# Kernel tuning notes

Hardware: AMD Instinct MI355X
Metric: run time of the kernel (lower is better)

The kernel has to match this reference:

```python
import jax, jax.numpy as jnp
import numpy as np

DEPTH = 4
HEADS = 8
DIM_HEAD = 32
NUM_CLUSTERS = 64
KMEANS_ITERS = 10
EPS = 1e-5


def layer_norm(x, g, b):
    m = jnp.mean(x, axis=-1, keepdims=True)
    v = jnp.var(x, axis=-1, keepdims=True)
    return (x - m) * jax.lax.rsqrt(v + EPS) * g + b


def kmeans_cluster(xf, k, iters):
    # xf: [P, D]. Lloyd's algorithm with deterministic init (first k points).
    centers = xf[:k]
    x_sq = jnp.sum(xf * xf, axis=-1, keepdims=True)  # [P,1]

    def assign(c):
        # squared distances [P, K]
        d = x_sq - 2.0 * (xf @ c.T) + jnp.sum(c * c, axis=-1)[None, :]
        return jnp.argmin(d, axis=-1)

    def step(c, _):
        labels = assign(c)
        sums = jax.ops.segment_sum(xf, labels, num_segments=k)
        counts = jax.ops.segment_sum(jnp.ones((xf.shape[0],), xf.dtype), labels, num_segments=k)
        new_c = jnp.where(counts[:, None] > 0, sums / jnp.maximum(counts, 1.0)[:, None], c)
        return new_c, None

    centers, _ = jax.lax.scan(step, centers, None, length=iters)
    labels = assign(centers)
    return centers[labels]  # gather: [P, D]


def setup_inputs() -> dict:
    key = jax.random.key(0)
    ks = jax.random.split(key, 8)
    B, N, D, L, M = 8, 1024, 256, DEPTH, 1024
    s = 0.02
    return {
        "x": jax.random.normal(ks[0], (B, N, D), jnp.float32),
        "ln1_g": jnp.ones((L, D), jnp.float32),
        "ln1_b": jnp.zeros((L, D), jnp.float32),
        "Wq": jax.random.normal(ks[1], (L, D, HEADS * DIM_HEAD), jnp.float32) * s,
        "Wkv": jax.random.normal(ks[2], (L, D, 2 * HEADS * DIM_HEAD), jnp.float32) * s,
        "Wo": jax.random.normal(ks[3], (L, HEADS * DIM_HEAD, D), jnp.float32) * s,
        "bo": jnp.zeros((L, D), jnp.float32),
        "ln2_g": jnp.ones((L, D), jnp.float32),
        "ln2_b": jnp.zeros((L, D), jnp.float32),
        "W1": jax.random.normal(ks[4], (L, D, M), jnp.float32) * s,
        "b1": jnp.zeros((L, M), jnp.float32),
        "W2": jax.random.normal(ks[5], (L, M, D), jnp.float32) * s,
        "b2": jnp.zeros((L, D), jnp.float32),
        "kW": jax.random.normal(ks[6], (D, D), jnp.float32) * s,
        "kb": jnp.zeros((D,), jnp.float32),
    }


def reference(x, ln1_g, ln1_b, Wq, Wkv, Wo, bo, ln2_g, ln2_b, W1, b1, W2, b2, kW, kb):
    B, N, D = x.shape
    h, dh = HEADS, DIM_HEAD
    scale = dh ** -0.5
    for l in range(DEPTH):
        # PreNorm self-attention + residual
        xn = layer_norm(x, ln1_g[l], ln1_b[l])
        q = (xn @ Wq[l]).reshape(B, N, h, dh)
        kv = xn @ Wkv[l]
        k, v = jnp.split(kv, 2, axis=-1)
        k = k.reshape(B, N, h, dh)
        v = v.reshape(B, N, h, dh)
        dots = jnp.einsum("bqhd,bkhd->bhqk", q, k) * scale
        attn = jax.nn.softmax(dots, axis=-1)
        out = jnp.einsum("bhqk,bkhd->bqhd", attn, v).reshape(B, N, h * dh)
        x = out @ Wo[l] + bo[l] + x
        # PreNorm FFN + residual
        xn = layer_norm(x, ln2_g[l], ln2_b[l])
        hdd = jax.nn.gelu(xn @ W1[l] + b1[l], approximate=False)
        x = hdd @ W2[l] + b2[l] + x
    # KMeans module: cluster flattened tokens, gather centers, linear transform.
    xf = x.reshape(B * N, D)
    clustered = kmeans_cluster(xf, NUM_CLUSTERS, KMEANS_ITERS)
    clustered = jax.lax.stop_gradient(clustered)  # torch detaches before sklearn
    clustered = clustered.reshape(B, N, D)
    return clustered @ kW + kb
```

## Files before the change

### kernel.cpp

```cpp
#include <hip/hip_runtime.h>
#include <hip/hip_bf16.h>
#include <math.h>

#define BN 8192
#define DMODEL 256
#define FFN 1024
#define NCLUST 64

typedef unsigned short u16;
typedef unsigned int u32;
typedef __attribute__((ext_vector_type(8))) short s16x8;
typedef __attribute__((ext_vector_type(8))) unsigned short u16x8;
typedef __attribute__((ext_vector_type(4))) unsigned short u16x4;
typedef __attribute__((ext_vector_type(4))) float f32x4;

__device__ __forceinline__ float bf2f(u16 v) {
    union { unsigned int u; float f; } w; w.u = ((unsigned int)v) << 16; return w.f;
}
__device__ __forceinline__ u16 f2bf(float f) {
    union { float f; unsigned int u; } w; w.f = f;
    unsigned int r = w.u + 0x7fffu + ((w.u >> 16) & 1u);
    return (u16)(r >> 16);
}
__device__ __forceinline__ u32 cvtpk(float lo, float hi) {
    u32 r;
    asm("v_cvt_pk_bf16_f32 %0, %1, %2" : "=v"(r) : "v"(lo), "v"(hi));
    return r;
}
__device__ __forceinline__ float u2f(u32 u) { union { u32 u; float f; } w; w.u = u; return w.f; }

__device__ __forceinline__ void gl16(const u16* g, u16* l) {
    __builtin_amdgcn_global_load_lds((const __attribute__((address_space(1))) u32*)g,
                                     (__attribute__((address_space(3))) u32*)l, 16, 0, 0);
}

#define BARRIER_LGKM() asm volatile("s_waitcnt lgkmcnt(0)\n\ts_barrier" ::: "memory")
#define MEMFENCE_ORDER() asm volatile("" ::: "memory")

__device__ __forceinline__ int sw32(int row, int col) { return row * 32 + (col ^ (((row >> 1) & 3) << 3)); }
__device__ __forceinline__ int sw64(int row, int col) { return row * 64 + (col ^ ((row & 7) << 3)); }
template<int BK>
__device__ __forceinline__ int swk(int row, int col) {
    if constexpr (BK == 32) return row * 32 + (col ^ (((row >> 1) & 3) << 3));
    else                    return row * 64 + (col ^ ((row & 7) << 3));
}

__global__ __launch_bounds__(256) void ln_wave(const float* __restrict__ x, const float* __restrict__ g,
                                               const float* __restrict__ b, u16* __restrict__ yh,
                                               u16* __restrict__ yl) {
    int t = threadIdx.x, w = t >> 6, l = t & 63;
    int row = blockIdx.x * 4 + w;
    const float* xr = x + (size_t)row * DMODEL;
    float4 v = *reinterpret_cast<const float4*>(xr + l * 4);
    float s = v.x + v.y + v.z + v.w;
    for (int off = 1; off < 64; off <<= 1) s += __shfl_xor(s, off);
    float mean = s * (1.0f / 256.0f);
    float4 dv = make_float4(v.x - mean, v.y - mean, v.z - mean, v.w - mean);
    float vs = dv.x * dv.x + dv.y * dv.y + dv.z * dv.z + dv.w * dv.w;
    for (int off = 1; off < 64; off <<= 1) vs += __shfl_xor(vs, off);
    float rs = rsqrtf(vs * (1.0f / 256.0f) + 1e-5f);
    float4 gg = *reinterpret_cast<const float4*>(g + l * 4);
    float4 bb = *reinterpret_cast<const float4*>(b + l * 4);
    float os[4] = {dv.x * rs * gg.x + bb.x, dv.y * rs * gg.y + bb.y,
                   dv.z * rs * gg.z + bb.z, dv.w * rs * gg.w + bb.w};
    u16x4 hv, lv;
#pragma unroll
    for (int j = 0; j < 4; j++) { u16 hh = f2bf(os[j]); hv[j] = hh; lv[j] = f2bf(os[j] - bf2f(hh)); }
    size_t o = (size_t)row * DMODEL + l * 4;
    *reinterpret_cast<u16x4*>(yh + o) = hv;
    *reinterpret_cast<u16x4*>(yl + o) = lv;
}

__device__ __forceinline__ void wconv_body(const float* __restrict__ W, u16* __restrict__ th,
                                           u16* __restrict__ tl, int K, int N, int bx, int by) {
    __shared__ float T[64][65];
    int k0 = by * 64, n0 = bx * 64;
    int t = threadIdx.x;
    int r = t >> 4, c4 = (t & 15) * 4;
#pragma unroll
    for (int i = 0; i < 4; i++) {
        float4 x = *reinterpret_cast<const float4*>(W + (size_t)(k0 + r + 16 * i) * N + n0 + c4);
        T[r + 16 * i][c4] = x.x; T[r + 16 * i][c4 + 1] = x.y;
        T[r + 16 * i][c4 + 2] = x.z; T[r + 16 * i][c4 + 3] = x.w;
    }
    __syncthreads();
#pragma unroll
    for (int i = 0; i < 4; i++) {
        int n = r + 16 * i;
        u16x4 h4, l4;
#pragma unroll
        for (int j = 0; j < 4; j++) {
            float v = T[c4 + j][n];
            u16 h = f2bf(v);
            h4[j] = h; l4[j] = f2bf(v - bf2f(h));
        }
        *reinterpret_cast<u16x4*>(th + (size_t)(n0 + n) * K + k0 + c4) = h4;
        *reinterpret_cast<u16x4*>(tl + (size_t)(n0 + n) * K + k0 + c4) = l4;
    }
}

__global__ __launch_bounds__(256) void wconv_all(const float* __restrict__ Wq, const float* __restrict__ Wkv,
                                                 const float* __restrict__ Wo, const float* __restrict__ W1,
                                                 const float* __restrict__ W2,
                                                 u16* __restrict__ wqkvh, u16* __restrict__ wqkvl,
                                                 u16* __restrict__ woh, u16* __restrict__ wol,
                                                 u16* __restrict__ w1h, u16* __restrict__ w1l,
                                                 u16* __restrict__ w2h, u16* __restrict__ w2l) {
    int f = blockIdx.x;
    if (f < 16)       wconv_body(Wq,  wqkvh,               wqkvl,               256, 256,  f & 3,  f >> 2);
    else if (f < 48)  { int g = f - 16;  wconv_body(Wkv, wqkvh + 65536,       wqkvl + 65536,       256, 512,  g & 7,  g >> 3); }
    else if (f < 64)  { int g = f - 48;  wconv_body(Wo,  woh,                 wol,                 256, 256,  g & 3,  g >> 2); }
    else if (f < 128) { int g = f - 64;  wconv_body(W1,  w1h,                 w1l,                 256, 1024, g & 15, g >> 4); }
    else              { int g = f - 128; wconv_body(W2,  w2h,                 w2l,                 1024, 256, g & 3,  g >> 2); }
}

template<int BM, int BNT, int BK>
__global__ __launch_bounds__(256) void gemm_t(const u16* __restrict__ Ath, const u16* __restrict__ Atl,
                                              const u16* __restrict__ Bth, const u16* __restrict__ Btl,
                                              const float* __restrict__ bias, const float* __restrict__ resid,
                                              float* __restrict__ Cf, u16* __restrict__ Ch, u16* __restrict__ Cl,
                                              int M, int N, int K, int fuse_gelu) {
    __shared__ u16 Ah[2][BM * BK], Al[2][BM * BK];
    __shared__ u16 Bh[2][BNT * BK], Bl[2][BNT * BK];
    constexpr int WAVES_N = (BM == 128 && BNT == 64) ? 1 : 2;
    constexpr int WAVES_M = 4 / WAVES_N;
    constexpr int MI = BM / (16 * WAVES_M);
    constexpr int NI = BNT / (16 * WAVES_N);
    constexpr int SEGS = (BM + BNT) * BK / 1024;
    constexpr int ROWS_SEG = 512 / BK;
    constexpr int ASEG = BM / ROWS_SEG;
    constexpr int BSEG = BNT / ROWS_SEG;
    int t = threadIdx.x;
    int m0 = blockIdx.y * BM, n0 = blockIdx.x * BNT;
    int L = t & 63, w = t >> 6, fr = L & 15, quad = L >> 4;
    int wm = (WAVES_N == 1) ? w : (w & 1);
    int wn = (WAVES_N == 1) ? 0 : (w >> 1);

    const u16* gsrc[SEGS];
    u16* ldst[SEGS];
    u32 dlt[SEGS];
    {
        int lr, lc;
        if constexpr (BK == 32) { lr = L >> 2; lc = (L & 3) * 8; }
        else                    { lr = L >> 3; lc = (L & 7) * 8; }
#pragma unroll
        for (int i = 0; i < SEGS; i++) {
            int s = w * SEGS + i;
            const u16* gb; u16* lb; int r; u32 d;
            if (s < ASEG)                 { gb = Ath + (size_t)m0 * K; lb = &Ah[0][0]; r = s * ROWS_SEG;                 d = BM * BK; }
            else if (s < 2 * ASEG)        { gb = Atl + (size_t)m0 * K; lb = &Al[0][0]; r = (s - ASEG) * ROWS_SEG;        d = BM * BK; }
            else if (s < 2 * ASEG + BSEG) { gb = Bth + (size_t)n0 * K; lb = &Bh[0][0]; r = (s - 2 * ASEG) * ROWS_SEG;    d = BNT * BK; }
            else                          { gb = Btl + (size_t)n0 * K; lb = &Bl[0][0]; r = (s - 2 * ASEG - BSEG) * ROWS_SEG; d = BNT * BK; }
            int row = r + lr;
            int scol;
            if constexpr (BK == 32) scol = lc ^ (((row >> 1) & 3) << 3);
            else                    scol = lc ^ ((row & 7) << 3);
            gsrc[i] = gb + (size_t)row * K + scol;
            ldst[i] = lb + r * BK;
            dlt[i] = d;
        }
    }

    f32x4 acc[MI][NI];
#pragma unroll
    for (int i = 0; i < MI; i++)
#pragma unroll
        for (int j = 0; j < NI; j++) acc[i][j] = (f32x4){0.0f, 0.0f, 0.0f, 0.0f};

    const int NT = K / BK;
#pragma unroll
    for (int i = 0; i < SEGS; i++) gl16(gsrc[i], ldst[i]);

    for (int tt = 0; tt < NT; tt++) {
        asm volatile("s_waitcnt lgkmcnt(0)" ::: "memory");
        __builtin_amdgcn_s_barrier();
        if (tt + 1 < NT) {
            int k0n = (tt + 1) * BK;
            u32 sel = (u32)((tt + 1) & 1);
#pragma unroll
            for (int i = 0; i < SEGS; i++) gl16(gsrc[i] + k0n, ldst[i] + sel * dlt[i]);
            asm volatile("s_waitcnt vmcnt(%0)" :: "n"(SEGS) : "memory");
        } else {
            asm volatile("s_waitcnt vmcnt(0)" ::: "memory");
        }
        __builtin_amdgcn_s_barrier();
        __builtin_amdgcn_sched_barrier(0);
        int cb = tt & 1;
        const u16* AhB = &Ah[cb][0]; const u16* AlB = &Al[cb][0];
        const u16* BhB = &Bh[cb][0]; const u16* BlB = &Bl[cb][0];
#pragma unroll
        for (int kk = 0; kk < BK / 32; kk++) {
            int kc = kk * 32 + quad * 8;
            s16x8 ah[MI], al[MI];
#pragma unroll
            for (int mi = 0; mi < MI; mi++) {
                int row = wm * (MI * 16) + mi * 16 + fr;
                ah[mi] = *reinterpret_cast<const s16x8*>(&AhB[swk<BK>(row, kc)]);
                al[mi] = *reinterpret_cast<const s16x8*>(&AlB[swk<BK>(row, kc)]);
            }
            __builtin_amdgcn_s_setprio(1);
#pragma unroll
            for (int ni = 0; ni < NI; ni++) {
                int rn = wn * (NI * 16) + ni * 16 + fr;
                s16x8 bhf = *reinterpret_cast<const s16x8*>(&BhB[swk<BK>(rn, kc)]);
                s16x8 blf = *reinterpret_cast<const s16x8*>(&BlB[swk<BK>(rn, kc)]);
#pragma unroll
                for (int mi = 0; mi < MI; mi++) {
                    acc[mi][ni] = __builtin_amdgcn_mfma_f32_16x16x32_bf16(ah[mi], bhf, acc[mi][ni], 0, 0, 0);
                    acc[mi][ni] = __builtin_amdgcn_mfma_f32_16x16x32_bf16(ah[mi], blf, acc[mi][ni], 0, 0, 0);
                    acc[mi][ni] = __builtin_amdgcn_mfma_f32_16x16x32_bf16(al[mi], bhf, acc[mi][ni], 0, 0, 0);
                }
            }
            __builtin_amdgcn_s_setprio(0);
        }
    }
#pragma unroll
    for (int mi = 0; mi < MI; mi++) {
#pragma unroll
        for (int ni = 0; ni < NI; ni++) {
#pragma unroll
            for (int r = 0; r < 4; r++) {
                int row = m0 + wm * (MI * 16) + mi * 16 + quad * 4 + r;
                int col = n0 + wn * (NI * 16) + ni * 16 + fr;
                float v = acc[mi][ni][r];
                if (bias) v += bias[col];
                if (fuse_gelu) v = 0.5f * v * (1.0f + erff(v * 0.70710678118654752f));
                if (resid) v += resid[(size_t)row * N + col];
                size_t o = (size_t)row * N + col;
                if (Cf) Cf[o] = v;
                if (Ch) { u16 hh = f2bf(v); Ch[o] = hh; Cl[o] = f2bf(v - bf2f(hh)); }
            }
        }
    }
}

__global__ __launch_bounds__(256) void attn14(const u16* __restrict__ qkvh, const u16* __restrict__ qkvl,
                                              u16* __restrict__ aoh, u16* __restrict__ aol) {
    int bh = blockIdx.x, b = bh >> 3, h = bh & 7;
    int qt = blockIdx.y;
    int t = threadIdx.x, L = t & 63, w = t >> 6;
    int fr = L & 15, quad = L >> 4;
    __shared__ u16 KH[2][64 * 32], KL[2][64 * 32];
    __shared__ u16 VTH[32 * 64], VTL[32 * 64];
    __shared__ u16 PH[4][16 * 64], PL[4][16 * 64];
    const float scale = 0.17677669529663687f;
    const int ROWS = 768;

    const u16* ksrc[2];
    u16* kdst[2];
    {
        int lr = L >> 2, lc = (L & 3) * 8;
#pragma unroll
        for (int i = 0; i < 2; i++) {
            int s = w * 2 + i;
            const u16* gb = (s < 4) ? qkvh : qkvl;
            u16* lb = (s < 4) ? &KH[0][0] : &KL[0][0];
            int r = (s & 3) * 16;
            int row = r + lr;
            int scol = lc ^ (((row >> 1) & 3) << 3);
            ksrc[i] = gb + ((size_t)(b * 1024) + row) * ROWS + 256 + h * 32 + scol;
            kdst[i] = lb + r * 32;
        }
    }

    size_t qoff0 = (size_t)(b * 1024 + qt * 128 + w * 16 + fr) * ROWS + h * 32 + quad * 8;
    s16x8 aqh0 = *reinterpret_cast<const s16x8*>(qkvh + qoff0);
    s16x8 aql0 = *reinterpret_cast<const s16x8*>(qkvl + qoff0);
    s16x8 aqh1 = *reinterpret_cast<const s16x8*>(qkvh + qoff0 + (size_t)64 * ROWS);
    s16x8 aql1 = *reinterpret_cast<const s16x8*>(qkvl + qoff0 + (size_t)64 * ROWS);

    int vp = t >> 3, vd0 = (t & 7) * 4;
    const u16* vh_ptr = qkvh + (size_t)(b * 1024 + 2 * vp) * ROWS + 512 + h * 32 + vd0;
    const u16* vl_ptr = qkvl + (size_t)(b * 1024 + 2 * vp) * ROWS + 512 + h * 32 + vd0;
    u16x4 vh0, vh1, vl0, vl1;
#define LOADV(kt_) do { size_t o_ = (size_t)((kt_) * 64) * ROWS;                                  \
        vh0 = *reinterpret_cast<const u16x4*>(vh_ptr + o_);                                       \
        vh1 = *reinterpret_cast<const u16x4*>(vh_ptr + o_ + ROWS);                                \
        vl0 = *reinterpret_cast<const u16x4*>(vl_ptr + o_);                                       \
        vl1 = *reinterpret_cast<const u16x4*>(vl_ptr + o_ + ROWS); } while (0)

    gl16(ksrc[0], kdst[0]);
    gl16(ksrc[1], kdst[1]);
    MEMFENCE_ORDER();
    LOADV(0);

    float m_0 = -1e30f, l_0 = 0.0f, m_1 = -1e30f, l_1 = 0.0f;
    f32x4 accA0, accA1, accB0, accB1;
    accA0 = (f32x4){0.0f, 0.0f, 0.0f, 0.0f}; accA1 = accA0; accB0 = accA0; accB1 = accA0;

#define SM_PV(SV, M_I, L_I, ACC0, ACC1) do {                                                      \
        float p[16];                                                                              \
        float ml = -1e30f;                                                                        \
        _Pragma("unroll")                                                                         \
        for (int ni = 0; ni < 4; ni++)                                                            \
            _Pragma("unroll")                                                                     \
            for (int r = 0; r < 4; r++) { float v = SV[ni][r] * scale; p[ni * 4 + r] = v; ml = fmaxf(ml, v); } \
        ml = fmaxf(ml, __shfl_xor(ml, 16));                                                       \
        ml = fmaxf(ml, __shfl_xor(ml, 32));                                                       \
        float mnew = fmaxf(M_I, ml);                                                              \
        float alpha = __expf(M_I - mnew);                                                         \
        M_I = mnew;                                                                               \
        float rs = 0.0f;                                                                          \
        _Pragma("unroll")                                                                         \
        for (int i = 0; i < 16; i++) { float e = __expf(p[i] - mnew); p[i] = e; rs += e; }        \
        rs += __shfl_xor(rs, 16);                                                                 \
        rs += __shfl_xor(rs, 32);                                                                 \
        L_I = L_I * alpha + rs;                                                                   \
        _Pragma("unroll")                                                                         \
        for (int ni = 0; ni < 4; ni++) {                                                          \
            float p0 = p[ni * 4], p1 = p[ni * 4 + 1], p2 = p[ni * 4 + 2], p3 = p[ni * 4 + 3];     \
            u32 qh01 = cvtpk(p0, p1), qh23 = cvtpk(p2, p3);                                       \
            float e0 = p0 - u2f(qh01 << 16);                                                      \
            float e1 = p1 - u2f(qh01 & 0xffff0000u);                                              \
            float e2 = p2 - u2f(qh23 << 16);                                                      \
            float e3 = p3 - u2f(qh23 & 0xffff0000u);                                              \
            u32 ql01 = cvtpk(e0, e1), ql23 = cvtpk(e2, e3);                                       \
            int c0 = sw64(fr, ni * 16 + quad * 4);                                                \
            int c1 = sw64(fr, ni * 16 + quad * 4 + 2);                                            \
            *reinterpret_cast<u32*>(&PH[w][c0]) = qh01;                                           \
            *reinterpret_cast<u32*>(&PH[w][c1]) = qh23;                                           \
            *reinterpret_cast<u32*>(&PL[w][c0]) = ql01;                                           \
            *reinterpret_cast<u32*>(&PL[w][c1]) = ql23;                                           \
        }                                                                                         \
        float a4[4];                                                                              \
        _Pragma("unroll")                                                                         \
        for (int r = 0; r < 4; r++) a4[r] = __shfl(alpha, quad * 4 + r);                          \
        ACC0[0] *= a4[0]; ACC0[1] *= a4[1]; ACC0[2] *= a4[2]; ACC0[3] *= a4[3];                   \
        ACC1[0] *= a4[0]; ACC1[1] *= a4[1]; ACC1[2] *= a4[2]; ACC1[3] *= a4[3];                   \
        __builtin_amdgcn_s_setprio(1);                                                            \
        _Pragma("unroll")                                                                         \
        for (int ks = 0; ks < 2; ks++) {                                                          \
            s16x8 aph = *reinterpret_cast<s16x8*>(&PH[w][sw64(fr, ks * 32 + quad * 8)]);          \
            s16x8 apl = *reinterpret_cast<s16x8*>(&PL[w][sw64(fr, ks * 32 + quad * 8)]);          \
            s16x8 bvh0 = *reinterpret_cast<s16x8*>(&VTH[sw64(fr, ks * 32 + quad * 8)]);           \
            s16x8 bvl0 = *reinterpret_cast<s16x8*>(&VTL[sw64(fr, ks * 32 + quad * 8)]);           \
            ACC0 = __builtin_amdgcn_mfma_f32_16x16x32_bf16(aph, bvh0, ACC0, 0, 0, 0);             \
            ACC0 = __builtin_amdgcn_mfma_f32_16x16x32_bf16(aph, bvl0, ACC0, 0, 0, 0);             \
            ACC0 = __builtin_amdgcn_mfma_f32_16x16x32_bf16(apl, bvh0, ACC0, 0, 0, 0);             \
            s16x8 bvh1 = *reinterpret_cast<s16x8*>(&VTH[sw64(16 + fr, ks * 32 + quad * 8)]);      \
            s16x8 bvl1 = *reinterpret_cast<s16x8*>(&VTL[sw64(16 + fr, ks * 32 + quad * 8)]);      \
            ACC1 = __builtin_amdgcn_mfma_f32_16x16x32_bf16(aph, bvh1, ACC1, 0, 0, 0);             \
            ACC1 = __builtin_amdgcn_mfma_f32_16x16x32_bf16(aph, bvl1, ACC1, 0, 0, 0);             \
            ACC1 = __builtin_amdgcn_mfma_f32_16x16x32_bf16(apl, bvh1, ACC1, 0, 0, 0);             \
        }                                                                                         \
        __builtin_amdgcn_s_setprio(0);                                                            \
    } while (0)

#pragma unroll 2
    for (int kt = 0; kt < 16; kt++) {
        int cur = kt & 1;
        BARRIER_LGKM();
        if (kt < 15) {
            size_t koff = (size_t)((kt + 1) * 64) * ROWS;
            u32 sel = (u32)((kt + 1) & 1) * (64 * 32);
            gl16(ksrc[0] + koff, kdst[0] + sel);
            gl16(ksrc[1] + koff, kdst[1] + sel);
        }
        {
#pragma unroll
            for (int i = 0; i < 4; i++) {
                int idx = sw64(vd0 + i, 2 * vp);
                *reinterpret_cast<u32*>(&VTH[idx]) = (u32)vh0[i] | ((u32)vh1[i] << 16);
                *reinterpret_cast<u32*>(&VTL[idx]) = (u32)vl0[i] | ((u32)vl1[i] << 16);
            }
        }
        BARRIER_LGKM();
        f32x4 sv0[4], sv1[4];
        __builtin_amdgcn_s_setprio(1);
#pragma unroll
        for (int ni = 0; ni < 4; ni++) {
            s16x8 bkh = *reinterpret_cast<s16x8*>(&KH[cur][sw32(ni * 16 + fr, quad * 8)]);
            s16x8 bkl = *reinterpret_cast<s16x8*>(&KL[cur][sw32(ni * 16 + fr, quad * 8)]);
            f32x4 c0 = (f32x4){0.0f, 0.0f, 0.0f, 0.0f};
            c0 = __builtin_amdgcn_mfma_f32_16x16x32_bf16(bkh, aqh0, c0, 0, 0, 0);
            c0 = __builtin_amdgcn_mfma_f32_16x16x32_bf16(bkl, aqh0, c0, 0, 0, 0);
            c0 = __builtin_amdgcn_mfma_f32_16x16x32_bf16(bkh, aql0, c0, 0, 0, 0);
            sv0[ni] = c0;
            f32x4 c1 = (f32x4){0.0f, 0.0f, 0.0f, 0.0f};
            c1 = __builtin_amdgcn_mfma_f32_16x16x32_bf16(bkh, aqh1, c1, 0, 0, 0);
            c1 = __builtin_amdgcn_mfma_f32_16x16x32_bf16(bkl, aqh1, c1, 0, 0, 0);
            c1 = __builtin_amdgcn_mfma_f32_16x16x32_bf16(bkh, aql1, c1, 0, 0, 0);
            sv1[ni] = c1;
        }
        __builtin_amdgcn_s_setprio(0);
        if (kt < 15) LOADV(kt + 1);
        SM_PV(sv0, m_0, l_0, accA0, accA1);
        SM_PV(sv1, m_1, l_1, accB0, accB1);
    }
#undef SM_PV
#undef LOADV
    float invl0 = 1.0f / l_0, invl1 = 1.0f / l_1;
#pragma unroll
    for (int r = 0; r < 4; r++) {
        float iv0 = __shfl(invl0, quad * 4 + r);
        float iv1 = __shfl(invl1, quad * 4 + r);
        size_t rb0 = ((size_t)(b * 1024 + qt * 128 + w * 16 + quad * 4 + r)) * DMODEL + h * 32;
        size_t rb1 = rb0 + (size_t)64 * DMODEL;
        float v0 = accA0[r] * iv0, v1 = accA1[r] * iv0;
        u16 h0 = f2bf(v0); aoh[rb0 + fr] = h0;      aol[rb0 + fr] = f2bf(v0 - bf2f(h0));
        u16 h1 = f2bf(v1); aoh[rb0 + 16 + fr] = h1; aol[rb0 + 16 + fr] = f2bf(v1 - bf2f(h1));
        float v2 = accB0[r] * iv1, v3 = accB1[r] * iv1;
        u16 h2 = f2bf(v2); aoh[rb1 + fr] = h2;      aol[rb1 + fr] = f2bf(v2 - bf2f(h2));
        u16 h3 = f2bf(v3); aoh[rb1 + 16 + fr] = h3; aol[rb1 + 16 + fr] = f2bf(v3 - bf2f(h3));
    }
}

__global__ __launch_bounds__(64) void csq_k(const float* __restrict__ centers, float* __restrict__ csq) {
    int j = blockIdx.x, l = threadIdx.x;
    float4 c4 = *reinterpret_cast<const float4*>(centers + j * DMODEL + l * 4);
    float s = c4.x * c4.x + c4.y * c4.y + c4.z * c4.z + c4.w * c4.w;
    for (int off = 1; off < 64; off <<= 1) s += __shfl_xor(s, off);
    if (l == 0) csq[j] = s;
}

__global__ __launch_bounds__(256) void km_distmin(const float* __restrict__ A, const float* __restrict__ Cn,
                                                  const float* __restrict__ csq, int* __restrict__ labels) {
    __shared__ float As[16][17];
    __shared__ float Bs[16][64];
    int t = threadIdx.x, tx = t & 15, ty = t >> 4;
    int m0 = blockIdx.x * 16;
    int mr = t >> 4, kq = t & 15;
    int jb = t & 63, kb = (t >> 6) * 4;
    float acc[4] = {};
    for (int k0 = 0; k0 < 256; k0 += 16) {
        __syncthreads();
        As[kq][mr] = A[(size_t)(m0 + mr) * DMODEL + k0 + kq];
        {
            float4 c4 = *reinterpret_cast<const float4*>(Cn + (size_t)jb * DMODEL + k0 + kb);
            Bs[kb][jb] = c4.x; Bs[kb + 1][jb] = c4.y; Bs[kb + 2][jb] = c4.z; Bs[kb + 3][jb] = c4.w;
        }
        __syncthreads();
#pragma unroll
        for (int kk = 0; kk < 16; kk++) {
            float a = As[kk][ty];
            float4 b4 = *reinterpret_cast<float4*>(&Bs[kk][tx * 4]);
            acc[0] += a * b4.x; acc[1] += a * b4.y; acc[2] += a * b4.z; acc[3] += a * b4.w;
        }
    }
    float4 cs4 = *reinterpret_cast<const float4*>(csq + tx * 4);
    float csv[4] = {cs4.x, cs4.y, cs4.z, cs4.w};
    float best = csv[0] - 2.0f * acc[0]; int bi = tx * 4;
#pragma unroll
    for (int j = 1; j < 4; j++) {
        float v = csv[j] - 2.0f * acc[j];
        if (v < best) { best = v; bi = tx * 4 + j; }
    }
    for (int off = 1; off < 16; off <<= 1) {
        float ov = __shfl_xor(best, off);
        int oi = __shfl_xor(bi, off);
        if (ov < best || (ov == best && oi < bi)) { best = ov; bi = oi; }
    }
    if (tx == 0) labels[m0 + ty] = bi;
}

__global__ __launch_bounds__(256) void km_segsum(const int* __restrict__ labels, const float* __restrict__ xf,
                                                 float* __restrict__ sums16, float* __restrict__ counts16) {
    int c = blockIdx.x, j = blockIdx.y, t = threadIdx.x;
    __shared__ int labs[512];
    if (t < 128) {
        int4 l4 = *reinterpret_cast<const int4*>(labels + c * 512 + t * 4);
        labs[t * 4] = l4.x; labs[t * 4 + 1] = l4.y; labs[t * 4 + 2] = l4.z; labs[t * 4 + 3] = l4.w;
    }
    __syncthreads();
    float acc = 0.0f, cnt = 0.0f;
    const float* xb = xf + (size_t)c * 512 * DMODEL;
    for (int i = 0; i < 512; i++) {
        if (labs[i] == j) { acc += xb[(size_t)i * DMODEL + t]; cnt += 1.0f; }
    }
    sums16[((size_t)c * NCLUST + j) * DMODEL + t] = acc;
    if (t == 0) counts16[c * NCLUST + j] = cnt;
}

__global__ __launch_bounds__(256) void km_update(float* __restrict__ centers, const float* __restrict__ sums16,
                                                 const float* __restrict__ counts16, float* __restrict__ csq) {
    __shared__ float red[256];
    int j = blockIdx.x, d = threadIdx.x;
    float c = 0.0f;
#pragma unroll
    for (int cc = 0; cc < 16; cc++) c += counts16[cc * NCLUST + j];
    float sv = 0.0f;
#pragma unroll
    for (int cc = 0; cc < 16; cc++) sv += sums16[((size_t)cc * NCLUST + j) * DMODEL + d];
    float cv = centers[j * DMODEL + d];
    if (c > 0.0f) cv = sv / fmaxf(c, 1.0f);
    centers[j * DMODEL + d] = cv;
    red[d] = cv * cv;
    __syncthreads();
    for (int off = 128; off; off >>= 1) { if (d < off) red[d] += red[d + off]; __syncthreads(); }
    if (d == 0) csq[j] = red[0];
}

__global__ __launch_bounds__(256) void nproj(const float* __restrict__ centers, const float* __restrict__ kW,
                                             const float* __restrict__ kb2, float* __restrict__ outc) {
    int idx = blockIdx.x * 256 + threadIdx.x;
    if (idx >= NCLUST * DMODEL) return;
    int row = idx >> 8, col = idx & 255;
    const float* cr = centers + row * DMODEL;
    float acc = 0.0f;
    for (int d = 0; d < DMODEL; d++) acc += cr[d] * kW[(size_t)d * DMODEL + col];
    outc[idx] = acc + kb2[col];
}

__global__ __launch_bounds__(256) void km_gather(const int* __restrict__ labels, const float* __restrict__ outc,
                                                 float* __restrict__ out) {
    int t = threadIdx.x;
#pragma unroll
    for (int r = 0; r < 4; r++) {
        int i = blockIdx.x * 4 + r;
        int lab = labels[i];
        out[(size_t)i * DMODEL + t] = outc[lab * DMODEL + t];
    }
}

extern "C" void kernel_launch(void* const* d_in, const int* in_sizes, int n_in,
                              void* d_out, int out_size, void* d_ws, size_t ws_size,
                              hipStream_t stream) {
    const float* x_in  = (const float*)d_in[0];
    const float* ln1_g = (const float*)d_in[1];
    const float* ln1_b = (const float*)d_in[2];
    const float* Wq    = (const float*)d_in[3];
    const float* Wkv   = (const float*)d_in[4];
    const float* Wo    = (const float*)d_in[5];
    const float* bo    = (const float*)d_in[6];
    const float* ln2_g = (const float*)d_in[7];
    const float* ln2_b = (const float*)d_in[8];
    const float* W1    = (const float*)d_in[9];
    const float* b1    = (const float*)d_in[10];
    const float* W2    = (const float*)d_in[11];
    const float* b2    = (const float*)d_in[12];
    const float* kWp   = (const float*)d_in[13];
    const float* kbp   = (const float*)d_in[14];
    float* out = (float*)d_out;

    const size_t NEEDED = 53477376;
    if (ws_size < NEEDED) {
        hipMemsetAsync(d_out, 0, (size_t)out_size * sizeof(float), stream);
        return;
    }

    char* ws = (char*)d_ws;
    float* xf      = (float*)(ws);
    u16*   xnh     = (u16*)  (ws + 8388608);
    u16*   xnl     = (u16*)  (ws + 12582912);
    u16*   aoh     = xnh;
    u16*   aol     = xnl;
    u16*   qkvh    = (u16*)  (ws + 16777216);
    u16*   qkvl    = (u16*)  (ws + 29360128);
    u16*   hbh     = (u16*)  (ws + 16777216);
    u16*   hbl     = (u16*)  (ws + 33554432);
    float* centers = (float*)(ws + 41943040);
    float* csqb    = (float*)(ws + 42008576);
    float* counts16= (float*)(ws + 42008832);
    int*   labels  = (int*)  (ws + 42012928);
    float* outc    = (float*)(ws + 42045696);
    float* sums16  = (float*)(ws + 42111232);
    u16*   wr      = (u16*)  (ws + 50331648);
    u16 *wqkvh = wr,          *wqkvl = wr + 196608;
    u16 *woh = wr + 393216,   *wol = wr + 458752;
    u16 *w1h = wr + 524288,   *w1l = wr + 786432;
    u16 *w2h = wr + 1048576,  *w2l = wr + 1310720;

    hipMemcpyAsync(xf, x_in, (size_t)BN * DMODEL * sizeof(float), hipMemcpyDeviceToDevice, stream);

    for (int l = 0; l < 4; l++) {
        wconv_all<<<192, 256, 0, stream>>>(Wq + (size_t)l * 65536, Wkv + (size_t)l * 131072,
                                           Wo + (size_t)l * 65536, W1 + (size_t)l * 262144,
                                           W2 + (size_t)l * 262144,
                                           wqkvh, wqkvl, woh, wol, w1h, w1l, w2h, w2l);

        ln_wave<<<BN / 4, 256, 0, stream>>>(xf, ln1_g + l * 256, ln1_b + l * 256, xnh, xnl);
        gemm_t<128, 128, 32><<<dim3(6, 64), 256, 0, stream>>>(xnh, xnl, wqkvh, wqkvl, nullptr, nullptr,
                                                              nullptr, qkvh, qkvl, BN, 768, 256, 0);
        attn14<<<dim3(64, 8), 256, 0, stream>>>(qkvh, qkvl, aoh, aol);
        gemm_t<64, 64, 64><<<dim3(4, 128), 256, 0, stream>>>(aoh, aol, woh, wol, bo + l * 256, xf,
                                                             xf, nullptr, nullptr, BN, 256, 256, 0);
        ln_wave<<<BN / 4, 256, 0, stream>>>(xf, ln2_g + l * 256, ln2_b + l * 256, xnh, xnl);
        gemm_t<128, 128, 32><<<dim3(8, 64), 256, 0, stream>>>(xnh, xnl, w1h, w1l, b1 + l * 1024, nullptr,
                                                              nullptr, hbh, hbl, BN, 1024, 256, 1);
        gemm_t<64, 64, 64><<<dim3(4, 128), 256, 0, stream>>>(hbh, hbl, w2h, w2l, b2 + l * 256, xf,
                                                             xf, nullptr, nullptr, BN, 256, 1024, 0);
    }

    hipMemcpyAsync(centers, xf, NCLUST * DMODEL * sizeof(float), hipMemcpyDeviceToDevice, stream);
    csq_k<<<64, 64, 0, stream>>>(centers, csqb);
    for (int it = 0; it < 10; it++) {
        km_distmin<<<512, 256, 0, stream>>>(xf, centers, csqb, labels);
        km_segsum<<<dim3(16, NCLUST), 256, 0, stream>>>(labels, xf, sums16, counts16);
        km_update<<<64, 256, 0, stream>>>(centers, sums16, counts16, csqb);
    }
    km_distmin<<<512, 256, 0, stream>>>(xf, centers, csqb, labels);
    nproj<<<64, 256, 0, stream>>>(centers, kWp, kbp, outc);
    km_gather<<<BN / 4, 256, 0, stream>>>(labels, outc, out);
}
```

Measured before the change: 1.253 ms.

## Swizzle GEMM block order and stage all centers in LDS for kmeans distance

The GEMM kernel remaps its linear workgroup index with a stride-8 swizzle, so workgroups scheduled near each other touch different tiles, aiming to spread work across XCDs and improve L2 locality. The kmeans distance kernel now loads all 64 centers (256x64 floats, padded) into shared memory once, then streams each row of A straight from global memory with float4 loads. This removes the 16 per-k-step barrier pairs. The cost is about 70KB of LDS per block, which cuts occupancy, and the swizzle assumes the workgroup count divides evenly by 8.

```diff
diff --git a/kernel.cpp b/kernel.cpp
--- a/kernel.cpp
+++ b/kernel.cpp
@@ -131,7 +131,12 @@
     constexpr int ASEG = BM / ROWS_SEG;
     constexpr int BSEG = BNT / ROWS_SEG;
     int t = threadIdx.x;
-    int m0 = blockIdx.y * BM, n0 = blockIdx.x * BNT;
+    int gx = gridDim.x;
+    int nwg = gx * gridDim.y;
+    int lin = blockIdx.y * gx + blockIdx.x;
+    int swz = (lin & 7) * (nwg >> 3) + (lin >> 3);
+    int bx = swz % gx, by = swz / gx;
+    int m0 = by * BM, n0 = bx * BNT;
     int L = t & 63, w = t >> 6, fr = L & 15, quad = L >> 4;
     int wm = (WAVES_N == 1) ? w : (w & 1);
     int wn = (WAVES_N == 1) ? 0 : (w >> 1);
@@ -415,27 +420,31 @@
 
 __global__ __launch_bounds__(256) void km_distmin(const float* __restrict__ A, const float* __restrict__ Cn,
                                                   const float* __restrict__ csq, int* __restrict__ labels) {
-    __shared__ float As[16][17];
-    __shared__ float Bs[16][64];
+    __shared__ float Cs[256][68];
     int t = threadIdx.x, tx = t & 15, ty = t >> 4;
     int m0 = blockIdx.x * 16;
-    int mr = t >> 4, kq = t & 15;
-    int jb = t & 63, kb = (t >> 6) * 4;
+    {
+        int j = t & 63, kc = (t >> 6) * 64;
+#pragma unroll
+        for (int i = 0; i < 16; i++) {
+            float4 c4 = *reinterpret_cast<const float4*>(Cn + (size_t)j * DMODEL + kc + i * 4);
+            Cs[kc + i * 4 + 0][j] = c4.x; Cs[kc + i * 4 + 1][j] = c4.y;
+            Cs[kc + i * 4 + 2][j] = c4.z; Cs[kc + i * 4 + 3][j] = c4.w;
+        }
+    }
+    __syncthreads();
+    const float* ar = A + (size_t)(m0 + ty) * DMODEL;
     float acc[4] = {};
-    for (int k0 = 0; k0 < 256; k0 += 16) {
-        __syncthreads();
-        As[kq][mr] = A[(size_t)(m0 + mr) * DMODEL + k0 + kq];
-        {
-            float4 c4 = *reinterpret_cast<const float4*>(Cn + (size_t)jb * DMODEL + k0 + kb);
-            Bs[kb][jb] = c4.x; Bs[kb + 1][jb] = c4.y; Bs[kb + 2][jb] = c4.z; Bs[kb + 3][jb] = c4.w;
-        }
-        __syncthreads();
-#pragma unroll
-        for (int kk = 0; kk < 16; kk++) {
-            float a = As[kk][ty];
-            float4 b4 = *reinterpret_cast<float4*>(&Bs[kk][tx * 4]);
-            acc[0] += a * b4.x; acc[1] += a * b4.y; acc[2] += a * b4.z; acc[3] += a * b4.w;
-        }
+    for (int kb = 0; kb < 64; kb++) {
+        float4 a4 = *reinterpret_cast<const float4*>(ar + kb * 4);
+        float4 b0 = *reinterpret_cast<float4*>(&Cs[kb * 4 + 0][tx * 4]);
+        float4 b1 = *reinterpret_cast<float4*>(&Cs[kb * 4 + 1][tx * 4]);
+        float4 b2 = *reinterpret_cast<float4*>(&Cs[kb * 4 + 2][tx * 4]);
+        float4 b3 = *reinterpret_cast<float4*>(&Cs[kb * 4 + 3][tx * 4]);
+        acc[0] += a4.x * b0.x; acc[1] += a4.x * b0.y; acc[2] += a4.x * b0.z; acc[3] += a4.x * b0.w;
+        acc[0] += a4.y * b1.x; acc[1] += a4.y * b1.y; acc[2] += a4.y * b1.z; acc[3] += a4.y * b1.w;
+        acc[0] += a4.z * b2.x; acc[1] += a4.z * b2.y; acc[2] += a4.z * b2.z; acc[3] += a4.z * b2.w;
+        acc[0] += a4.w * b3.x; acc[1] += a4.w * b3.y; acc[2] += a4.w * b3.z; acc[3] += a4.w * b3.w;
     }
     float4 cs4 = *reinterpret_cast<const float4*>(csq + tx * 4);
     float csv[4] = {cs4.x, cs4.y, cs4.z, cs4.w};
```

After: 1.226 ms. -2.1%, faster.
